# Kernel optimization log

Hardware: AMD Instinct MI355X
Metric: run time of the kernel (lower is better)

## Reference

```python
import jax, jax.numpy as jnp
from jax import lax
import numpy as np

STRIDES = (2, 2)
PADDING = 'SAME'
EPS = 1e-05


def setup_inputs() -> dict:
    key = jax.random.key(0)
    k1, k2, k3 = jax.random.split(key, 3)
    x = jax.random.normal(k1, (16, 64, 64, 256), dtype=jnp.float32)
    # flax default conv kernel init ~ lecun_normal; plain normal scaled is fine for a math reference
    kernel = jax.random.normal(k2, (4, 4, 256, 128), dtype=jnp.float32) * 0.05
    bias = jax.random.normal(k3, (128,), dtype=jnp.float32) * 0.01
    alpha = jnp.ones((1,), dtype=jnp.float32)
    return {'x': x, 'kernel': kernel, 'bias': bias, 'alpha': alpha}


def reference(x, kernel, bias, alpha):
    # x: [B, H, W, Cin] NHWC; kernel: [kh, kw, Cin, Cout]
    out_features = kernel.shape[-1]

    # main transposed conv: dot-product map  [B, H*2, W*2, Cout]
    dot = lax.conv_transpose(x, kernel, STRIDES, PADDING, transpose_kernel=False)

    # patch squared-sum map: conv_transpose of x**2 with an all-ones kernel
    # of shape kernel_size + (Cin, 1); broadcast over Cout (same math as jnp.repeat)
    ones_k = jnp.ones(kernel.shape[:-1] + (1,), dtype=kernel.dtype)
    patch_sq = lax.conv_transpose(x * x, ones_k, STRIDES, PADDING, transpose_kernel=False)  # [B, H', W', 1]

    # per-filter kernel squared norm, reduced over (kh, kw, Cin) -> [Cout]
    k_sq = jnp.sum(kernel * kernel, axis=(0, 1, 2))

    # ||x_patch - W||^2 = sum(x^2) + sum(W^2) - 2 * <x, W>
    dist_sq = patch_sq + k_sq - 2.0 * dot

    y = (dot * dot) / (dist_sq + EPS)
    y = y + bias  # broadcast over [B, H', W', Cout]

    nf = jnp.float32(out_features)
    scale = (jnp.sqrt(nf) / jnp.log1p(nf)) ** alpha  # alpha shape (1,) broadcasts
    return y * scale
```

## Files before the change

### kernel.cpp

```cpp
#include <hip/hip_runtime.h>
#include <cstdint>
#include <cstddef>

#define CIN   256
#define COUT  128

typedef float  f32x4  __attribute__((ext_vector_type(4)));
typedef __bf16 bf16x8 __attribute__((ext_vector_type(8)));
typedef unsigned int u32x4 __attribute__((ext_vector_type(4)));

#define XF_BYTES   (16ull*66*32*66*8*2)
#define WF_OFF     XF_BYTES
#define WF_BYTES   (16ull*8*4*128*8*2)
#define SPAD_OFF   (WF_OFF + WF_BYTES)
#define SPAD_BYTES (16ull*66*66*4)
#define KSQ_OFF    (SPAD_OFF + SPAD_BYTES)
#define WS_NEEDED  (KSQ_OFF + 512)

__device__ __forceinline__ unsigned short f2bf(float f) {
  unsigned int u = __float_as_uint(f);
  u += 0x7fffu + ((u >> 16) & 1u);
  return (unsigned short)(u >> 16);
}

__global__ __launch_bounds__(256) void prep_x2(
    const float* __restrict__ x, unsigned short* __restrict__ xf,
    float* __restrict__ spad)
{
  __shared__ __align__(16) unsigned short lw[66*258 + 8];
  int blk = blockIdx.x;
  int b = blk / 66, row = blk - b*66;
  int t = threadIdx.x, wave = t >> 6, lane = t & 63;
  bool interior = (row >= 1 && row <= 64);
  int iy = row - 1;

  if (interior) {
    #pragma unroll
    for (int p = 0; p < 16; ++p) {
      int cx = 4*p + wave;
      f32x4 v = *(const f32x4*)(x + (((size_t)b*64 + iy)*64 + cx)*CIN + lane*4);
      ushort4 h; h.x=f2bf(v.x); h.y=f2bf(v.y); h.z=f2bf(v.z); h.w=f2bf(v.w);
      *(ushort4*)&lw[(size_t)(cx+1)*258 + lane*4] = h;
      float s = v.x*v.x + v.y*v.y + v.z*v.z + v.w*v.w;
      #pragma unroll
      for (int off = 32; off > 0; off >>= 1) s += __shfl_down(s, off);
      if (lane == 0) spad[(size_t)blk*66 + cx + 1] = s;
    }
    if (t < 2) spad[(size_t)blk*66 + t*65] = 0.f;
    if (t < 64) {
      int col = (t & 1) * 65, q = t >> 1;
      *(uint4*)&lw[(size_t)col*258 + q*8] = (uint4){0,0,0,0};
    }
  } else {
    if (t < 66) spad[(size_t)blk*66 + t] = 0.f;
  }
  __syncthreads();

  size_t obase = (size_t)blk * 32 * 66 * 8;
  #pragma unroll
  for (int k = 0; k < 9; ++k) {
    int un = k*256 + t;
    if (un < 2112) {
      int q = un / 66, col = un - q*66;
      uint4 val = interior ? *(uint4*)&lw[(size_t)col*258 + q*8]
                           : (uint4){0u,0u,0u,0u};
      *(uint4*)(xf + obase + (size_t)un*8) = val;
    }
  }
}

__global__ __launch_bounds__(256) void prep_w2(
    const float* __restrict__ w, unsigned short* __restrict__ wf,
    float* __restrict__ ksq)
{
  int blk = blockIdx.x;
  int tap = blk >> 3, c8 = blk & 7;
  int t = threadIdx.x;
  #pragma unroll
  for (int rr = 0; rr < 2; ++rr) {
    int row = rr*256 + t;
    int q = row >> 7, co = row & 127;
    float s = 0.f;
    union { unsigned short u[8]; uint4 v; } hh;
    #pragma unroll
    for (int e = 0; e < 8; ++e) {
      int ci = c8*32 + q*8 + e;
      float v = w[((size_t)tap*256 + ci)*COUT + co];
      s += v*v;
      hh.u[e] = f2bf(v);
    }
    *(uint4*)(wf + ((size_t)blk*4 + q)*128*8 + (size_t)co*8) = hh.v;
    atomicAdd(ksq + co, s);
  }
}

__global__ __launch_bounds__(256, 2) void yat_main(
    const unsigned short* __restrict__ xf,
    const unsigned short* __restrict__ wf,
    const float* __restrict__ spad,
    const float* __restrict__ ksq,
    const float* __restrict__ bias,
    const float* __restrict__ alpha,
    float* __restrict__ out)
{
  __shared__ float srow[132];

  int orig = blockIdx.x;
  int bid = (orig & 7) * 256 + (orig >> 3);
  int py = bid & 1, u = (bid >> 1) & 63, b = bid >> 7;
  int t = threadIdx.x, wave = t >> 6, lane = t & 63;
  int px = wave >> 1, coh = wave & 1;
  int l15 = lane & 15, l4 = lane >> 4;

  if (t < 132) {
    int r = t / 66, c = t - r*66;
    srow[t] = spad[((size_t)b*66 + (u + py) + r)*66 + c];
  }

  const unsigned short* ab =
      xf + ((((size_t)b*66 + (u + py))*32 + l4)*66 + px + l15)*8;
  const unsigned short* wb =
      wf + ((size_t)l4*128 + coh*64 + l15)*8 + (size_t)(py*4 + px)*32768;

  f32x4 acc[4][4];
  #pragma unroll
  for (int i = 0; i < 4; ++i)
    #pragma unroll
    for (int j = 0; j < 4; ++j)
      acc[i][j] = (f32x4){0.f, 0.f, 0.f, 0.f};

  u32x4 Aq0[2][4], Bq0[2][4], Aq1[2][4], Bq1[2][4];

#define GL(dst, base, off)                                                 \
  asm volatile("global_load_dwordx4 %0, %1, off offset:%c2"                \
               : "=v"(dst) : "v"(base), "i"(off))

#define ISSUE(SUF, AA, C8)                                                 \
  {                                                                        \
    const char* pa  = (const char*)ab + (AA)*33792 + (C8)*4224;            \
    const char* pb0 = (const char*)wb + (AA)*524288 + (C8)*8192;           \
    const char* pb1 = pb0 + 131072;                                        \
    GL(Aq##SUF[0][0], pa, 0);   GL(Aq##SUF[0][1], pa, 256);                \
    GL(Aq##SUF[0][2], pa, 512); GL(Aq##SUF[0][3], pa, 768);                \
    GL(Aq##SUF[1][0], pa, 16);  GL(Aq##SUF[1][1], pa, 272);                \
    GL(Aq##SUF[1][2], pa, 528); GL(Aq##SUF[1][3], pa, 784);                \
    GL(Bq##SUF[0][0], pb0, 0);   GL(Bq##SUF[0][1], pb0, 256);              \
    GL(Bq##SUF[0][2], pb0, 512); GL(Bq##SUF[0][3], pb0, 768);              \
    GL(Bq##SUF[1][0], pb1, 0);   GL(Bq##SUF[1][1], pb1, 256);              \
    GL(Bq##SUF[1][2], pb1, 512); GL(Bq##SUF[1][3], pb1, 768);              \
  }

#define MFMA32(SUF)                                                        \
  {                                                                        \
    __builtin_amdgcn_s_setprio(1);                                         \
    _Pragma("unroll")                                                      \
    for (int bb = 0; bb < 2; ++bb)                                         \
      _Pragma("unroll")                                                    \
      for (int mt = 0; mt < 4; ++mt)                                       \
        _Pragma("unroll")                                                  \
        for (int nt = 0; nt < 4; ++nt)                                     \
          acc[mt][nt] = __builtin_amdgcn_mfma_f32_16x16x32_bf16(           \
              __builtin_bit_cast(bf16x8, Aq##SUF[bb][mt]),                 \
              __builtin_bit_cast(bf16x8, Bq##SUF[bb][nt]),                 \
              acc[mt][nt], 0, 0, 0);                                       \
    __builtin_amdgcn_s_setprio(0);                                         \
  }

#define SB __builtin_amdgcn_sched_barrier(0)
#define VMW(N) do { asm volatile("s_waitcnt vmcnt(" #N ")" ::: "memory");  \
                    SB; } while (0)

  ISSUE(0, 0, 0); SB;

  #pragma unroll
  for (int c8 = 0; c8 < 8; ++c8) {
    ISSUE(1, 1, c8); SB;
    VMW(16);
    MFMA32(0); SB;
    if (c8 < 7) { ISSUE(0, 0, c8 + 1); SB; VMW(16); }
    else        { VMW(0); }
    MFMA32(1); SB;
  }

#undef GL
#undef ISSUE
#undef MFMA32
#undef VMW
#undef SB

  __syncthreads();

  float scale = powf(sqrtf(128.f) / log1pf(128.f), alpha[0]);
  int oy = 2*u + py;
  float kq[4], bi[4];
  #pragma unroll
  for (int nt = 0; nt < 4; ++nt) {
    int n = coh*64 + nt*16 + l15;
    kq[nt] = ksq[n]; bi[nt] = bias[n];
  }
  size_t orow = ((size_t)b*128 + oy) * 128 * COUT;
  #pragma unroll
  for (int mt = 0; mt < 4; ++mt) {
    #pragma unroll
    for (int r = 0; r < 4; ++r) {
      int v = mt*16 + l4*4 + r;
      float ps = srow[v+px] + srow[v+px+1] + srow[66 + v+px] + srow[66 + v+px+1];
      #pragma unroll
      for (int nt = 0; nt < 4; ++nt) {
        float dot = acc[mt][nt][r];
        float dist = ps + kq[nt] - 2.f*dot + 1e-5f;
        float y = (dot*dot/dist + bi[nt]) * scale;
        int n = coh*64 + nt*16 + l15;
        out[orow + (size_t)(2*v + px)*COUT + n] = y;
      }
    }
  }
}

__global__ __launch_bounds__(256) void fb_ksq(const float* __restrict__ w,
                                              float* __restrict__ ksq) {
  __shared__ float red[256];
  int co = blockIdx.x, t = threadIdx.x;
  float s = 0.f;
  for (int j = t; j < 4096; j += 256) { float v = w[(size_t)j*COUT + co]; s += v*v; }
  red[t] = s; __syncthreads();
  for (int off = 128; off > 0; off >>= 1) {
    if (t < off) red[t] += red[t + off];
    __syncthreads();
  }
  if (t == 0) ksq[co] = red[0];
}

__global__ __launch_bounds__(256) void fb_main(
    const float* __restrict__ x, const float* __restrict__ w,
    const float* __restrict__ bias, const float* __restrict__ alpha,
    const float* __restrict__ ksq, float* __restrict__ out)
{
  size_t idx = (size_t)blockIdx.x * 256 + threadIdx.x;
  int co = (int)(idx & 127);
  int ox = (int)((idx >> 7) & 127);
  int oy = (int)((idx >> 14) & 127);
  int b  = (int)(idx >> 21);
  int py = oy & 1, px = ox & 1, u = oy >> 1, v = ox >> 1;
  float dot = 0.f, ps = 0.f;
  for (int a = 0; a < 2; ++a) {
    int iy = u + py + a - 1;
    if (iy < 0 || iy > 63) continue;
    for (int b2 = 0; b2 < 2; ++b2) {
      int ix = v + px + b2 - 1;
      if (ix < 0 || ix > 63) continue;
      const float* xp = x + (((size_t)b*64 + iy)*64 + ix)*CIN;
      const float* wp = w + ((size_t)((py + 2*a)*4 + (px + 2*b2))*CIN)*COUT + co;
      for (int ci = 0; ci < CIN; ++ci) {
        float xv = xp[ci];
        dot += xv * wp[(size_t)ci*COUT];
        ps  += xv * xv;
      }
    }
  }
  float dist = ps + ksq[co] - 2.f*dot + 1e-5f;
  float scale = powf(sqrtf(128.f) / log1pf(128.f), alpha[0]);
  out[idx] = (dot*dot/dist + bias[co]) * scale;
}

extern "C" void kernel_launch(void* const* d_in, const int* in_sizes, int n_in,
                              void* d_out, int out_size, void* d_ws, size_t ws_size,
                              hipStream_t stream)
{
  const float* x     = (const float*)d_in[0];
  const float* w     = (const float*)d_in[1];
  const float* bias  = (const float*)d_in[2];
  const float* alpha = (const float*)d_in[3];
  float* out = (float*)d_out;

  if (ws_size < WS_NEEDED) {
    float* ksq = (float*)d_ws;
    fb_ksq<<<128, 256, 0, stream>>>(w, ksq);
    fb_main<<<131072, 256, 0, stream>>>(x, w, bias, alpha, ksq, out);
    return;
  }

  unsigned short* xfp = (unsigned short*)d_ws;
  unsigned short* wfp = (unsigned short*)((char*)d_ws + WF_OFF);
  float* spad = (float*)((char*)d_ws + SPAD_OFF);
  float* ksq  = (float*)((char*)d_ws + KSQ_OFF);

  hipMemsetAsync(ksq, 0, 512, stream);
  prep_x2<<<1056, 256, 0, stream>>>(x, xfp, spad);
  prep_w2<<<128, 256, 0, stream>>>(w, wfp, ksq);
  yat_main<<<2048, 256, 0, stream>>>(xfp, wfp, spad, ksq, bias, alpha, out);
}
```

Before: 118.0 us.

## Switch main kernel to 32x32x16 MFMA with two output rows per block

The main kernel now computes two output rows of the same parity per block, using 32x32x16 bf16 MFMAs. It reuses three loaded input rows across both output rows and all four taps, which cuts the global loads of activation data per MFMA. The activation and weight layouts are reorganized into 16-channel groups to match the new MFMA operand shape. The kernel-norm sum moves from atomics in the weight prep to the separate reduction kernel, and occupancy drops to one block per CU because of the larger register use.

```diff
diff --git a/kernel.cpp b/kernel.cpp
--- a/kernel.cpp
+++ b/kernel.cpp
@@ -6,13 +6,14 @@
 #define COUT  128
 
 typedef float  f32x4  __attribute__((ext_vector_type(4)));
+typedef float  f32x16 __attribute__((ext_vector_type(16)));
 typedef __bf16 bf16x8 __attribute__((ext_vector_type(8)));
 typedef unsigned int u32x4 __attribute__((ext_vector_type(4)));
 
-#define XF_BYTES   (16ull*66*32*66*8*2)
-#define WF_OFF     XF_BYTES
-#define WF_BYTES   (16ull*8*4*128*8*2)
-#define SPAD_OFF   (WF_OFF + WF_BYTES)
+#define XG_BYTES   (16ull*66*16*66*16*2)
+#define WG_OFF     XG_BYTES
+#define WG_BYTES   (16ull*16*128*16*2)
+#define SPAD_OFF   (WG_OFF + WG_BYTES)
 #define SPAD_BYTES (16ull*66*66*4)
 #define KSQ_OFF    (SPAD_OFF + SPAD_BYTES)
 #define WS_NEEDED  (KSQ_OFF + 512)
@@ -23,11 +24,11 @@
   return (unsigned short)(u >> 16);
 }
 
-__global__ __launch_bounds__(256) void prep_x2(
-    const float* __restrict__ x, unsigned short* __restrict__ xf,
+__global__ __launch_bounds__(256) void prep_x3(
+    const float* __restrict__ x, unsigned short* __restrict__ xg,
     float* __restrict__ spad)
 {
-  __shared__ __align__(16) unsigned short lw[66*258 + 8];
+  __shared__ __align__(16) unsigned short lw[66*258];
   int blk = blockIdx.x;
   int b = blk / 66, row = blk - b*66;
   int t = threadIdx.x, wave = t >> 6, lane = t & 63;
@@ -47,173 +48,45 @@
       if (lane == 0) spad[(size_t)blk*66 + cx + 1] = s;
     }
     if (t < 2) spad[(size_t)blk*66 + t*65] = 0.f;
-    if (t < 64) {
-      int col = (t & 1) * 65, q = t >> 1;
-      *(uint4*)&lw[(size_t)col*258 + q*8] = (uint4){0,0,0,0};
+    if (t < 128) {
+      int col = (t & 1) * 65, i = t >> 1;
+      *(ushort4*)&lw[(size_t)col*258 + i*4] = (ushort4){0,0,0,0};
     }
   } else {
     if (t < 66) spad[(size_t)blk*66 + t] = 0.f;
   }
   __syncthreads();
 
-  size_t obase = (size_t)blk * 32 * 66 * 8;
-  #pragma unroll
-  for (int k = 0; k < 9; ++k) {
+  size_t obase = (size_t)blk * 16896;
+  #pragma unroll
+  for (int k = 0; k < 5; ++k) {
     int un = k*256 + t;
-    if (un < 2112) {
-      int q = un / 66, col = un - q*66;
-      uint4 val = interior ? *(uint4*)&lw[(size_t)col*258 + q*8]
-                           : (uint4){0u,0u,0u,0u};
-      *(uint4*)(xf + obase + (size_t)un*8) = val;
-    }
-  }
-}
-
-__global__ __launch_bounds__(256) void prep_w2(
-    const float* __restrict__ w, unsigned short* __restrict__ wf,
-    float* __restrict__ ksq)
-{
-  int blk = blockIdx.x;
-  int tap = blk >> 3, c8 = blk & 7;
+    if (un < 1056) {
+      int cc = un / 66, col = un - cc*66;
+      uint4 v0 = {0,0,0,0}, v1 = {0,0,0,0};
+      if (interior) {
+        v0 = *(uint4*)&lw[(size_t)col*258 + cc*16];
+        v1 = *(uint4*)&lw[(size_t)col*258 + cc*16 + 8];
+      }
+      *(uint4*)(xg + obase + (size_t)un*16) = v0;
+      *(uint4*)(xg + obase + (size_t)un*16 + 8) = v1;
+    }
+  }
+}
+
+__global__ __launch_bounds__(256) void prep_w3(
+    const float* __restrict__ w, unsigned short* __restrict__ wg)
+{
+  int tap = blockIdx.x;
   int t = threadIdx.x;
-  #pragma unroll
-  for (int rr = 0; rr < 2; ++rr) {
-    int row = rr*256 + t;
-    int q = row >> 7, co = row & 127;
-    float s = 0.f;
+  int co = t & 127, kh = t >> 7;
+  #pragma unroll
+  for (int cc = 0; cc < 16; ++cc) {
     union { unsigned short u[8]; uint4 v; } hh;
     #pragma unroll
-    for (int e = 0; e < 8; ++e) {
-      int ci = c8*32 + q*8 + e;
-      float v = w[((size_t)tap*256 + ci)*COUT + co];
-      s += v*v;
-      hh.u[e] = f2bf(v);
-    }
-    *(uint4*)(wf + ((size_t)blk*4 + q)*128*8 + (size_t)co*8) = hh.v;
-    atomicAdd(ksq + co, s);
-  }
-}
-
-__global__ __launch_bounds__(256, 2) void yat_main(
-    const unsigned short* __restrict__ xf,
-    const unsigned short* __restrict__ wf,
-    const float* __restrict__ spad,
-    const float* __restrict__ ksq,
-    const float* __restrict__ bias,
-    const float* __restrict__ alpha,
-    float* __restrict__ out)
-{
-  __shared__ float srow[132];
-
-  int orig = blockIdx.x;
-  int bid = (orig & 7) * 256 + (orig >> 3);
-  int py = bid & 1, u = (bid >> 1) & 63, b = bid >> 7;
-  int t = threadIdx.x, wave = t >> 6, lane = t & 63;
-  int px = wave >> 1, coh = wave & 1;
-  int l15 = lane & 15, l4 = lane >> 4;
-
-  if (t < 132) {
-    int r = t / 66, c = t - r*66;
-    srow[t] = spad[((size_t)b*66 + (u + py) + r)*66 + c];
-  }
-
-  const unsigned short* ab =
-      xf + ((((size_t)b*66 + (u + py))*32 + l4)*66 + px + l15)*8;
-  const unsigned short* wb =
-      wf + ((size_t)l4*128 + coh*64 + l15)*8 + (size_t)(py*4 + px)*32768;
-
-  f32x4 acc[4][4];
-  #pragma unroll
-  for (int i = 0; i < 4; ++i)
-    #pragma unroll
-    for (int j = 0; j < 4; ++j)
-      acc[i][j] = (f32x4){0.f, 0.f, 0.f, 0.f};
-
-  u32x4 Aq0[2][4], Bq0[2][4], Aq1[2][4], Bq1[2][4];
-
-#define GL(dst, base, off)                                                 \
-  asm volatile("global_load_dwordx4 %0, %1, off offset:%c2"                \
-               : "=v"(dst) : "v"(base), "i"(off))
-
-#define ISSUE(SUF, AA, C8)                                                 \
-  {                                                                        \
-    const char* pa  = (const char*)ab + (AA)*33792 + (C8)*4224;            \
-    const char* pb0 = (const char*)wb + (AA)*524288 + (C8)*8192;           \
-    const char* pb1 = pb0 + 131072;                                        \
-    GL(Aq##SUF[0][0], pa, 0);   GL(Aq##SUF[0][1], pa, 256);                \
-    GL(Aq##SUF[0][2], pa, 512); GL(Aq##SUF[0][3], pa, 768);                \
-    GL(Aq##SUF[1][0], pa, 16);  GL(Aq##SUF[1][1], pa, 272);                \
-    GL(Aq##SUF[1][2], pa, 528); GL(Aq##SUF[1][3], pa, 784);                \
-    GL(Bq##SUF[0][0], pb0, 0);   GL(Bq##SUF[0][1], pb0, 256);              \
-    GL(Bq##SUF[0][2], pb0, 512); GL(Bq##SUF[0][3], pb0, 768);              \
-    GL(Bq##SUF[1][0], pb1, 0);   GL(Bq##SUF[1][1], pb1, 256);              \
-    GL(Bq##SUF[1][2], pb1, 512); GL(Bq##SUF[1][3], pb1, 768);              \
-  }
-
-#define MFMA32(SUF)                                                        \
-  {                                                                        \
-    __builtin_amdgcn_s_setprio(1);                                         \
-    _Pragma("unroll")                                                      \
-    for (int bb = 0; bb < 2; ++bb)                                         \
-      _Pragma("unroll")                                                    \
-      for (int mt = 0; mt < 4; ++mt)                                       \
-        _Pragma("unroll")                                                  \
-        for (int nt = 0; nt < 4; ++nt)                                     \
-          acc[mt][nt] = __builtin_amdgcn_mfma_f32_16x16x32_bf16(           \
-              __builtin_bit_cast(bf16x8, Aq##SUF[bb][mt]),                 \
-              __builtin_bit_cast(bf16x8, Bq##SUF[bb][nt]),                 \
-              acc[mt][nt], 0, 0, 0);                                       \
-    __builtin_amdgcn_s_setprio(0);                                         \
-  }
-
-#define SB __builtin_amdgcn_sched_barrier(0)
-#define VMW(N) do { asm volatile("s_waitcnt vmcnt(" #N ")" ::: "memory");  \
-                    SB; } while (0)
-
-  ISSUE(0, 0, 0); SB;
-
-  #pragma unroll
-  for (int c8 = 0; c8 < 8; ++c8) {
-    ISSUE(1, 1, c8); SB;
-    VMW(16);
-    MFMA32(0); SB;
-    if (c8 < 7) { ISSUE(0, 0, c8 + 1); SB; VMW(16); }
-    else        { VMW(0); }
-    MFMA32(1); SB;
-  }
-
-#undef GL
-#undef ISSUE
-#undef MFMA32
-#undef VMW
-#undef SB
-
-  __syncthreads();
-
-  float scale = powf(sqrtf(128.f) / log1pf(128.f), alpha[0]);
-  int oy = 2*u + py;
-  float kq[4], bi[4];
-  #pragma unroll
-  for (int nt = 0; nt < 4; ++nt) {
-    int n = coh*64 + nt*16 + l15;
-    kq[nt] = ksq[n]; bi[nt] = bias[n];
-  }
-  size_t orow = ((size_t)b*128 + oy) * 128 * COUT;
-  #pragma unroll
-  for (int mt = 0; mt < 4; ++mt) {
-    #pragma unroll
-    for (int r = 0; r < 4; ++r) {
-      int v = mt*16 + l4*4 + r;
-      float ps = srow[v+px] + srow[v+px+1] + srow[66 + v+px] + srow[66 + v+px+1];
-      #pragma unroll
-      for (int nt = 0; nt < 4; ++nt) {
-        float dot = acc[mt][nt][r];
-        float dist = ps + kq[nt] - 2.f*dot + 1e-5f;
-        float y = (dot*dot/dist + bi[nt]) * scale;
-        int n = coh*64 + nt*16 + l15;
-        out[orow + (size_t)(2*v + px)*COUT + n] = y;
-      }
-    }
+    for (int e = 0; e < 8; ++e)
+      hh.u[e] = f2bf(w[((size_t)tap*256 + cc*16 + kh*8 + e)*COUT + co]);
+    *(uint4*)(wg + (((size_t)tap*16 + cc)*128 + co)*16 + kh*8) = hh.v;
   }
 }
 
@@ -229,6 +102,172 @@
     __syncthreads();
   }
   if (t == 0) ksq[co] = red[0];
+}
+
+__global__ __launch_bounds__(256, 1) void yat_main(
+    const unsigned short* __restrict__ xg,
+    const unsigned short* __restrict__ wg,
+    const float* __restrict__ spad,
+    const float* __restrict__ ksq,
+    const float* __restrict__ bias,
+    const float* __restrict__ alpha,
+    float* __restrict__ out)
+{
+  __shared__ float srow[198];
+
+  int orig = blockIdx.x;
+  int bid = (orig & 7) * 128 + (orig >> 3);
+  int py = bid & 1, u2 = (bid >> 1) & 31, b = bid >> 6;
+  int t = threadIdx.x, wave = t >> 6, lane = t & 63;
+  int px = wave >> 1, coh = wave & 1;
+  int l31 = lane & 31, hi = lane >> 5;
+  int base = 2*u2 + py;
+
+  if (t < 198) {
+    int r = t / 66, c = t - r*66;
+    srow[t] = spad[((size_t)b*66 + base + r)*66 + c];
+  }
+  asm volatile("s_waitcnt vmcnt(0) lgkmcnt(0)" ::: "memory");
+  __syncthreads();
+
+  const char* paB = (const char*)xg
+      + ((size_t)(b*66 + base))*33792
+      + (size_t)(px + l31)*32 + hi*16;
+  const char* pa0 = paB;
+  const char* pa1 = paB + 33792;
+  const char* pa2 = paB + 67584;
+  const char* pbB = (const char*)wg + (size_t)(coh*64 + l31)*32 + hi*16;
+  const char* pb00 = pbB + (size_t)((py    )*4 + px    )*65536;
+  const char* pb01 = pbB + (size_t)((py    )*4 + px + 2)*65536;
+  const char* pb10 = pbB + (size_t)((py + 2)*4 + px    )*65536;
+  const char* pb11 = pbB + (size_t)((py + 2)*4 + px + 2)*65536;
+
+  f32x16 acc[2][2][2];
+  #pragma unroll
+  for (int j = 0; j < 2; ++j)
+    #pragma unroll
+    for (int v = 0; v < 2; ++v)
+      #pragma unroll
+      for (int n = 0; n < 2; ++n)
+        #pragma unroll
+        for (int e = 0; e < 16; ++e)
+          acc[j][v][n][e] = 0.f;
+
+  u32x4 A0[12], A1[12];
+  u32x4 B0[8],  B1[8];
+
+#define SB __builtin_amdgcn_sched_barrier(0)
+#define VMW(N) do { asm volatile("s_waitcnt vmcnt(" #N ")" ::: "memory"); SB; } while (0)
+#define GLB(dst, base, off)                                                \
+  asm volatile("global_load_dwordx4 %0, %1, off offset:%c2"                \
+               : "=v"(dst) : "v"(base), "i"(off))
+
+#define ISSUE_A(BK)                                                        \
+  {                                                                        \
+    GLB(BK[0],  pa0, 0);  GLB(BK[1],  pa0, 32);                            \
+    GLB(BK[2],  pa0, 1024); GLB(BK[3],  pa0, 1056);                        \
+    GLB(BK[4],  pa1, 0);  GLB(BK[5],  pa1, 32);                            \
+    GLB(BK[6],  pa1, 1024); GLB(BK[7],  pa1, 1056);                        \
+    GLB(BK[8],  pa2, 0);  GLB(BK[9],  pa2, 32);                            \
+    GLB(BK[10], pa2, 1024); GLB(BK[11], pa2, 1056);                        \
+  }
+
+#define ISSUE_B(BK)                                                        \
+  {                                                                        \
+    GLB(BK[0], pb00, 0); GLB(BK[1], pb00, 1024);                           \
+    GLB(BK[2], pb01, 0); GLB(BK[3], pb01, 1024);                           \
+    GLB(BK[4], pb10, 0); GLB(BK[5], pb10, 1024);                           \
+    GLB(BK[6], pb11, 0); GLB(BK[7], pb11, 1024);                           \
+  }
+
+#define ADV                                                                \
+  { pa0 += 2112; pa1 += 2112; pa2 += 2112;                                 \
+    pb00 += 4096; pb01 += 4096; pb10 += 4096; pb11 += 4096; }
+
+#define MFMA32(A_, B_)                                                     \
+  {                                                                        \
+    _Pragma("unroll")                                                      \
+    for (int a = 0; a < 2; ++a)                                            \
+      _Pragma("unroll")                                                    \
+      for (int bb = 0; bb < 2; ++bb)                                       \
+        _Pragma("unroll")                                                  \
+        for (int j = 0; j < 2; ++j)                                        \
+          _Pragma("unroll")                                                \
+          for (int vh = 0; vh < 2; ++vh)                                   \
+            _Pragma("unroll")                                              \
+            for (int nt = 0; nt < 2; ++nt)                                 \
+              acc[j][vh][nt] = __builtin_amdgcn_mfma_f32_32x32x16_bf16(    \
+                  __builtin_bit_cast(bf16x8, A_[(j+a)*4 + vh*2 + bb]),     \
+                  __builtin_bit_cast(bf16x8, B_[a*4 + bb*2 + nt]),         \
+                  acc[j][vh][nt], 0, 0, 0);                                \
+  }
+
+#define STEP_FULL(A_, B_) { VMW(20); MFMA32(A_, B_); SB;                   \
+                            ISSUE_A(A_); ISSUE_B(B_); SB; ADV; SB; }
+#define STEP_T1(A_, B_)   { VMW(20); MFMA32(A_, B_); SB; }
+#define STEP_T0(A_, B_)   { VMW(0);  MFMA32(A_, B_); SB; }
+
+  ISSUE_A(A0); ISSUE_B(B0); SB; ADV; SB;
+  ISSUE_A(A1); ISSUE_B(B1); SB; ADV; SB;
+
+  STEP_FULL(A0, B0);
+  STEP_FULL(A1, B1);
+  STEP_FULL(A0, B0);
+  STEP_FULL(A1, B1);
+  STEP_FULL(A0, B0);
+  STEP_FULL(A1, B1);
+  STEP_FULL(A0, B0);
+  STEP_FULL(A1, B1);
+  STEP_FULL(A0, B0);
+  STEP_FULL(A1, B1);
+  STEP_FULL(A0, B0);
+  STEP_FULL(A1, B1);
+  STEP_FULL(A0, B0);
+  STEP_FULL(A1, B1);
+  STEP_T1(A0, B0);
+  STEP_T0(A1, B1);
+
+#undef SB
+#undef VMW
+#undef GLB
+#undef ISSUE_A
+#undef ISSUE_B
+#undef ADV
+#undef MFMA32
+#undef STEP_FULL
+#undef STEP_T1
+#undef STEP_T0
+
+  float scale = powf(sqrtf(128.f) / log1pf(128.f), alpha[0]);
+  float kq[2], bi[2];
+  #pragma unroll
+  for (int nt = 0; nt < 2; ++nt) {
+    int n = coh*64 + nt*32 + l31;
+    kq[nt] = ksq[n]; bi[nt] = bias[n];
+  }
+  #pragma unroll
+  for (int j = 0; j < 2; ++j) {
+    int oy = 4*u2 + 2*j + py;
+    size_t orow = ((size_t)b*128 + oy) * 128 * COUT;
+    #pragma unroll
+    for (int vh = 0; vh < 2; ++vh) {
+      #pragma unroll
+      for (int reg = 0; reg < 16; ++reg) {
+        int rowid = (reg & 3) + 8*(reg >> 2) + 4*hi;
+        int v = vh*32 + rowid;
+        float ps = srow[j*66 + v+px] + srow[j*66 + v+px+1]
+                 + srow[(j+1)*66 + v+px] + srow[(j+1)*66 + v+px+1];
+        #pragma unroll
+        for (int nt = 0; nt < 2; ++nt) {
+          float dot = acc[j][vh][nt][reg];
+          float dist = ps + kq[nt] - 2.f*dot + 1e-5f;
+          float y = (dot*dot/dist + bi[nt]) * scale;
+          int n = coh*64 + nt*32 + l31;
+          out[orow + (size_t)(2*v + px)*COUT + n] = y;
+        }
+      }
+    }
+  }
 }
 
 __global__ __launch_bounds__(256) void fb_main(
@@ -280,13 +319,13 @@
     return;
   }
 
-  unsigned short* xfp = (unsigned short*)d_ws;
-  unsigned short* wfp = (unsigned short*)((char*)d_ws + WF_OFF);
+  unsigned short* xgp = (unsigned short*)d_ws;
+  unsigned short* wgp = (unsigned short*)((char*)d_ws + WG_OFF);
   float* spad = (float*)((char*)d_ws + SPAD_OFF);
   float* ksq  = (float*)((char*)d_ws + KSQ_OFF);
 
-  hipMemsetAsync(ksq, 0, 512, stream);
-  prep_x2<<<1056, 256, 0, stream>>>(x, xfp, spad);
-  prep_w2<<<128, 256, 0, stream>>>(w, wfp, ksq);
-  yat_main<<<2048, 256, 0, stream>>>(xfp, wfp, spad, ksq, bias, alpha, out);
-}
+  fb_ksq<<<128, 256, 0, stream>>>(w, ksq);
+  prep_x3<<<1056, 256, 0, stream>>>(x, xgp, spad);
+  prep_w3<<<16, 256, 0, stream>>>(w, wgp);
+  yat_main<<<1024, 256, 0, stream>>>(xgp, wgp, spad, ksq, bias, alpha, out);
+}
```

Result: no change. 119.8 us (+1.5%).
